# Kernel tuning notes

Measured on AMD Instinct MI355X. Metric: run time of the kernel, lower is better.

Reference implementation:

```python
import jax, jax.numpy as jnp
import numpy as np

B, TM1, ENC, DEC, OUT = 256, 32, 128, 128, 1


def setup_inputs() -> dict:
    key = jax.random.key(0)
    ks = jax.random.split(key, 16)
    s = 0.05
    inp = {
        "input_encoded": jax.random.normal(ks[0], (B, TM1, ENC), jnp.float32),
        "y_history": jax.random.normal(ks[1], (B, TM1, OUT), jnp.float32),
        # attn_layer: Linear(2*DEC+ENC -> ENC), Tanh, Linear(ENC -> 1)
        "attn_W1": jax.random.normal(ks[2], (ENC, 2 * DEC + ENC), jnp.float32) * s,
        "attn_b1": jnp.zeros((ENC,), jnp.float32),
        "attn_W2": jax.random.normal(ks[3], (1, ENC), jnp.float32) * s,
        "attn_b2": jnp.zeros((1,), jnp.float32),
        # LSTM(input_size=OUT, hidden_size=DEC), pytorch gate order i,f,g,o
        "W_ih": jax.random.normal(ks[4], (4 * DEC, OUT), jnp.float32) * s,
        "W_hh": jax.random.normal(ks[5], (4 * DEC, DEC), jnp.float32) * s,
        "b_ih": jnp.zeros((4 * DEC,), jnp.float32),
        "b_hh": jnp.zeros((4 * DEC,), jnp.float32),
        # fc: Linear(ENC+OUT -> OUT), weight initialized with normal_() in torch
        "fc_W": jax.random.normal(ks[6], (OUT, ENC + OUT), jnp.float32),
        "fc_b": jnp.zeros((OUT,), jnp.float32),
        # fc_final: Linear(DEC+ENC -> OUT)
        "fcf_W": jax.random.normal(ks[7], (OUT, DEC + ENC), jnp.float32) * s,
        "fcf_b": jnp.zeros((OUT,), jnp.float32),
    }
    return inp


def _forward(input_encoded, y_history, attn_W1, attn_b1, attn_W2, attn_b2,
             W_ih, W_hh, b_ih, b_hh, fc_W, fc_b, fcf_W, fcf_b):
    b, tm1, enc = input_encoded.shape
    dec = W_hh.shape[1]

    h0 = jnp.zeros((b, dec), input_encoded.dtype)
    c0 = jnp.zeros((b, dec), input_encoded.dtype)
    ctx0 = jnp.zeros((b, enc), input_encoded.dtype)

    def step(carry, y_t):  # y_t: [B, OUT]
        h, c, _ = carry
        hc = jnp.concatenate([h, c], axis=-1)  # [B, 2*DEC]
        x = jnp.concatenate(
            [jnp.broadcast_to(hc[:, None, :], (b, tm1, 2 * dec)), input_encoded],
            axis=-1)  # [B, T-1, 2*DEC+ENC]
        hdn = jnp.tanh(jnp.einsum('bte,he->bth', x, attn_W1) + attn_b1)
        logits = jnp.einsum('bth,oh->bto', hdn, attn_W2)[..., 0] + attn_b2[0]  # [B, T-1]
        attn = jax.nn.softmax(logits, axis=1)
        ctx = jnp.einsum('bt,bte->be', attn, input_encoded)  # [B, ENC]
        y_tilde = jnp.concatenate([ctx, y_t], axis=1) @ fc_W.T + fc_b  # [B, OUT]
        gates = y_tilde @ W_ih.T + b_ih + h @ W_hh.T + b_hh  # [B, 4*DEC]
        i, f, g, o = jnp.split(gates, 4, axis=-1)
        c_new = jax.nn.sigmoid(f) * c + jax.nn.sigmoid(i) * jnp.tanh(g)
        h_new = jax.nn.sigmoid(o) * jnp.tanh(c_new)
        return (h_new, c_new, ctx), None

    (h, c, ctx), _ = jax.lax.scan(step, (h0, c0, ctx0),
                                  jnp.swapaxes(y_history, 0, 1))
    out = jnp.concatenate([h, ctx], axis=1) @ fcf_W.T + fcf_b + y_history[:, -1]
    return out  # [B, OUT]


def reference(input_encoded, y_history, attn_W1, attn_b1, attn_W2, attn_b2,
              W_ih, W_hh, b_ih, b_hh, fc_W, fc_b, fcf_W, fcf_b):
    return _forward(input_encoded, y_history, attn_W1, attn_b1, attn_W2, attn_b2,
                    W_ih, W_hh, b_ih, b_hh, fc_W, fc_b, fcf_W, fcf_b)
```

## Files before the change

### kernel.cpp

```cpp
#include <hip/hip_runtime.h>


#define TT 32

typedef _Float16 h2_t __attribute__((ext_vector_type(2)));
typedef _Float16 h4_t __attribute__((ext_vector_type(4)));
typedef _Float16 h8_t __attribute__((ext_vector_type(8)));

#if __has_builtin(__builtin_amdgcn_fdot2)
#define FDOT2(a, b, c) __builtin_amdgcn_fdot2((a), (b), (c), false)
#else
static __device__ __forceinline__ float FDOT2(h2_t a, h2_t b, float c) {
    return c + (float)a[0] * (float)b[0] + (float)a[1] * (float)b[1];
}
#endif

__device__ __forceinline__ float dot_h8(h8_t w, h8_t v, float acc) {
    acc = FDOT2(__builtin_shufflevector(w, w, 0, 1), __builtin_shufflevector(v, v, 0, 1), acc);
    acc = FDOT2(__builtin_shufflevector(w, w, 2, 3), __builtin_shufflevector(v, v, 2, 3), acc);
    acc = FDOT2(__builtin_shufflevector(w, w, 4, 5), __builtin_shufflevector(v, v, 4, 5), acc);
    acc = FDOT2(__builtin_shufflevector(w, w, 6, 7), __builtin_shufflevector(v, v, 6, 7), acc);
    return acc;
}
__device__ __forceinline__ h8_t pk8(float4 a, float4 b) {
    h8_t r;
    r[0] = (_Float16)a.x; r[1] = (_Float16)a.y; r[2] = (_Float16)a.z; r[3] = (_Float16)a.w;
    r[4] = (_Float16)b.x; r[5] = (_Float16)b.y; r[6] = (_Float16)b.z; r[7] = (_Float16)b.w;
    return r;
}
__device__ __forceinline__ float fast_tanh(float x) {
    float e = __expf(2.f * x);
    return 1.f - __fdividef(2.f, e + 1.f);
}
__device__ __forceinline__ float fast_sig(float x) {
    return __fdividef(1.f, 1.f + __expf(-x));
}

__global__ __launch_bounds__(1024, 4) void decoder_kernel(
    const float* __restrict__ enc_g,
    const float* __restrict__ yh_g,
    const float* __restrict__ W1,
    const float* __restrict__ b1,
    const float* __restrict__ W2,
    const float* __restrict__ b2,
    const float* __restrict__ Wih,
    const float* __restrict__ Whh,
    const float* __restrict__ bih,
    const float* __restrict__ bhh,
    const float* __restrict__ fcW,
    const float* __restrict__ fcB,
    const float* __restrict__ fcfW,
    const float* __restrict__ fcfB,
    float* __restrict__ out)
{
    __shared__ __align__(16) h8_t s_whh8[512 * 16];
    __shared__ __align__(16) _Float16 s_enc16[TT * 136];
    __shared__ __align__(16) _Float16 s_epre16[TT * 128];
    __shared__ __align__(16) _Float16 s_hcx[4 * 272];
    __shared__ __align__(16) _Float16 s_A16[128];
    __shared__ __align__(16) _Float16 s_w216[128];
    __shared__ __align__(16) float s_gdot[512];
    __shared__ __align__(16) _Float16 s_wih16[512];
    __shared__ float s_logit[TT];
    __shared__ float s_q[TT];
    __shared__ float s_att[TT];
    __shared__ float s_yh[TT];
    __shared__ float s_ctx[128];

    const int tid = threadIdx.x;
    const int b = blockIdx.x;
    const int lane = tid & 63;

    {
        const float4* encp = (const float4*)(enc_g + (size_t)b * TT * 128);
        float4 v = encp[tid];
        int t = tid >> 5, e4 = tid & 31;
        h4_t hv;
        hv[0] = (_Float16)v.x; hv[1] = (_Float16)v.y;
        hv[2] = (_Float16)v.z; hv[3] = (_Float16)v.w;
        *(h4_t*)(s_enc16 + t * 136 + e4 * 4) = hv;
    }
    if (tid < 544) ((unsigned int*)s_hcx)[tid] = 0u;
    if (tid < 128) s_w216[tid] = (_Float16)W2[tid];
    if (tid < TT) s_yh[tid] = yh_g[b * TT + tid];

    float bias_r = 0.f;
    h8_t w1a[8];
    if (tid < 512) {
        const int r = tid, rx = r & 15;
        const float4* wp = (const float4*)(Whh + (size_t)r * 128);
#pragma unroll
        for (int c = 0; c < 16; c++)
            s_whh8[(r << 4) | (c ^ rx)] = pk8(wp[2 * c], wp[2 * c + 1]);
        s_wih16[r] = (_Float16)Wih[r];
        bias_r = bih[r] + bhh[r];
    } else {
        const int u = tid - 512, g = u >> 2, s4 = u & 3;
        const float4* p = (const float4*)(W1 + g * 384 + s4 * 64);
#pragma unroll
        for (int k = 0; k < 8; k++) w1a[k] = pk8(p[2 * k], p[2 * k + 1]);
    }
    const float b2v = b2[0];
    const float fcw128 = fcW[128];
    const float fcbv = fcB[0];
    const float fcfbv = fcfB[0];
    __syncthreads();

    {
        const int g8 = tid >> 3, s8 = tid & 7;
        const float4* wp = (const float4*)(W1 + g8 * 384 + 256 + s8 * 16);
        h8_t wa = pk8(wp[0], wp[1]);
        h8_t wb = pk8(wp[2], wp[3]);
        const float b1v = b1[g8];
        for (int t = 0; t < TT; t++) {
            const h8_t* ep8 = (const h8_t*)(s_enc16 + t * 136);
            float pa = dot_h8(wa, ep8[s8 * 2], 0.f);
            pa = dot_h8(wb, ep8[s8 * 2 + 1], pa);
            pa += __shfl_xor(pa, 1);
            pa += __shfl_xor(pa, 2);
            pa += __shfl_xor(pa, 4);
            if (s8 == 0) s_epre16[t * 128 + g8] = (_Float16)(pa + b1v);
        }
    }
    if (tid < 256) {
        const int t = tid >> 3, s8 = tid & 7;
        const float4* fp = (const float4*)(fcW + s8 * 16);
        h8_t fa = pk8(fp[0], fp[1]);
        h8_t fb = pk8(fp[2], fp[3]);
        const h8_t* ep8 = (const h8_t*)(s_enc16 + t * 136);
        float pq = dot_h8(fa, ep8[s8 * 2], 0.f);
        pq = dot_h8(fb, ep8[s8 * 2 + 1], pq);
        pq += __shfl_xor(pq, 1);
        pq += __shfl_xor(pq, 2);
        pq += __shfl_xor(pq, 4);
        if (s8 == 0) s_q[t] = pq;
    }
    h8_t w8wih;
    float c0r = 0.f, c1r = 0.f;
    if (tid >= 512 && tid < 576) {
#pragma unroll
        for (int j = 0; j < 8; j++) w8wih[j] = s_wih16[j * 64 + lane];
    }
    __syncthreads();

    const h8_t* hcp8 = (const h8_t*)s_hcx;

#define GDOT(c, acc) acc = dot_h8(s_whh8[base | ((c) ^ rx)], hcp8[(c)], acc)

    for (int t = 0; t < TT; t++) {
        float pg0 = 0.f, pg1 = 0.f;
        if (tid < 512) {
            const int rx = tid & 15, base = tid << 4;
            GDOT(0, pg0); GDOT(1, pg1); GDOT(2, pg0); GDOT(3, pg1);
            GDOT(4, pg0); GDOT(5, pg1); GDOT(6, pg0); GDOT(7, pg1);
        } else {
            const int u = tid - 512, g = u >> 2, s4 = u & 3;
            const h8_t* hp = (const h8_t*)(s_hcx + s4 * 272);
            float a0 = 0.f, a1 = 0.f;
#pragma unroll
            for (int k = 0; k < 8; k += 2) {
                a0 = dot_h8(w1a[k], hp[s4 * 8 + k], a0);
                a1 = dot_h8(w1a[k + 1], hp[s4 * 8 + k + 1], a1);
            }
            float aa = a0 + a1;
            aa += __shfl_xor(aa, 1);
            aa += __shfl_xor(aa, 2);
            if (s4 == 0) s_A16[g] = (_Float16)aa;
        }
        __syncthreads();

        if (tid < 512) {
            const int rx = tid & 15, base = tid << 4;
            GDOT(8, pg0); GDOT(9, pg1); GDOT(10, pg0); GDOT(11, pg1);
            GDOT(12, pg0); GDOT(13, pg1); GDOT(14, pg0); GDOT(15, pg1);
            s_gdot[tid] = pg0 + pg1 + bias_r;
        } else {
            const int u = tid - 512, tt_ = u >> 4, sub = u & 15;
            h8_t ev = ((const h8_t*)(s_epre16 + tt_ * 128))[sub];
            h8_t av = ((const h8_t*)s_A16)[sub];
            h8_t wv = ((const h8_t*)s_w216)[sub];
            float lp = 0.f;
#pragma unroll
            for (int i = 0; i < 8; i++)
                lp += (float)wv[i] * fast_tanh((float)av[i] + (float)ev[i]);
            lp += __shfl_xor(lp, 1);
            lp += __shfl_xor(lp, 2);
            lp += __shfl_xor(lp, 4);
            lp += __shfl_xor(lp, 8);
            if (sub == 0) s_logit[tt_] = lp + b2v;
        }
        __syncthreads();

        if (tid >= 512 && tid < 576) {
            float el = 0.f, ql = 0.f;
            if (lane < TT) { el = __expf(s_logit[lane]); ql = s_q[lane]; }
            float ss = el, ys = el * ql;
#pragma unroll
            for (int m = 1; m < 64; m <<= 1) {
                ss += __shfl_xor(ss, m);
                ys += __shfl_xor(ys, m);
            }
            float inv = __fdividef(1.f, ss);
            if (lane < TT) s_att[lane] = el * inv;
            float yt = ys * inv + fcw128 * s_yh[t] + fcbv;
            float g0 = s_gdot[lane]       + (float)w8wih[0] * yt;
            float g1 = s_gdot[64 + lane]  + (float)w8wih[1] * yt;
            float g2 = s_gdot[128 + lane] + (float)w8wih[2] * yt;
            float g3 = s_gdot[192 + lane] + (float)w8wih[3] * yt;
            float g4 = s_gdot[256 + lane] + (float)w8wih[4] * yt;
            float g5 = s_gdot[320 + lane] + (float)w8wih[5] * yt;
            float g6 = s_gdot[384 + lane] + (float)w8wih[6] * yt;
            float g7 = s_gdot[448 + lane] + (float)w8wih[7] * yt;
            float cn0 = fast_sig(g2) * c0r + fast_sig(g0) * fast_tanh(g4);
            float cn1 = fast_sig(g3) * c1r + fast_sig(g1) * fast_tanh(g5);
            float hn0 = fast_sig(g6) * fast_tanh(cn0);
            float hn1 = fast_sig(g7) * fast_tanh(cn1);
            c0r = cn0; c1r = cn1;
            _Float16 h0 = (_Float16)hn0, h1 = (_Float16)hn1;
            _Float16 cc0 = (_Float16)cn0, cc1 = (_Float16)cn1;
#pragma unroll
            for (int j = 0; j < 4; j++) {
                _Float16* bp = s_hcx + j * 272;
                bp[lane] = h0;
                bp[64 + lane] = h1;
                bp[128 + lane] = cc0;
                bp[192 + lane] = cc1;
            }
        }
        __syncthreads();
    }
#undef GDOT

    if (tid < 128) {
        float acc = 0.f;
#pragma unroll 8
        for (int t = 0; t < TT; t++) acc += s_att[t] * (float)s_enc16[t * 136 + tid];
        s_ctx[tid] = acc;
    }
    __syncthreads();
    if (tid < 64) {
        float p = fcfW[lane] * (float)s_hcx[lane] +
                  fcfW[64 + lane] * (float)s_hcx[64 + lane] +
                  fcfW[128 + lane] * s_ctx[lane] +
                  fcfW[192 + lane] * s_ctx[64 + lane];
#pragma unroll
        for (int m = 1; m < 64; m <<= 1) p += __shfl_xor(p, m);
        if (lane == 0) out[b] = p + fcfbv + s_yh[TT - 1];
    }
}

extern "C" void kernel_launch(void* const* d_in, const int* in_sizes, int n_in,
                              void* d_out, int out_size, void* d_ws, size_t ws_size,
                              hipStream_t stream) {
    decoder_kernel<<<256, 1024, 0, stream>>>(
        (const float*)d_in[0], (const float*)d_in[1], (const float*)d_in[2],
        (const float*)d_in[3], (const float*)d_in[4], (const float*)d_in[5],
        (const float*)d_in[6], (const float*)d_in[7], (const float*)d_in[8],
        (const float*)d_in[9], (const float*)d_in[10], (const float*)d_in[11],
        (const float*)d_in[12], (const float*)d_in[13], (float*)d_out);
}
```

Before: 173.8 us.

## Halve block size, keep W_hh in registers, spread LSTM gate activations

Measured after the change: 173.6 us. About the same (-0.1%).

```diff
diff --git a/kernel.cpp b/kernel.cpp
--- a/kernel.cpp
+++ b/kernel.cpp
@@ -36,7 +36,7 @@
     return __fdividef(1.f, 1.f + __expf(-x));
 }
 
-__global__ __launch_bounds__(1024, 4) void decoder_kernel(
+__global__ __launch_bounds__(512, 2) void decoder_kernel(
     const float* __restrict__ enc_g,
     const float* __restrict__ yh_g,
     const float* __restrict__ W1,
@@ -53,14 +53,13 @@
     const float* __restrict__ fcfB,
     float* __restrict__ out)
 {
-    __shared__ __align__(16) h8_t s_whh8[512 * 16];
+    __shared__ __align__(16) h8_t s_w1a8[512 * 8];
     __shared__ __align__(16) _Float16 s_enc16[TT * 136];
     __shared__ __align__(16) _Float16 s_epre16[TT * 128];
-    __shared__ __align__(16) _Float16 s_hcx[4 * 272];
+    __shared__ __align__(16) _Float16 s_hc[2 * 272];
     __shared__ __align__(16) _Float16 s_A16[128];
     __shared__ __align__(16) _Float16 s_w216[128];
-    __shared__ __align__(16) float s_gdot[512];
-    __shared__ __align__(16) _Float16 s_wih16[512];
+    __shared__ __align__(16) float s_act[512];
     __shared__ float s_logit[TT];
     __shared__ float s_q[TT];
     __shared__ float s_att[TT];
@@ -70,35 +69,40 @@
     const int tid = threadIdx.x;
     const int b = blockIdx.x;
     const int lane = tid & 63;
+    const int g1 = tid >> 2, s4 = tid & 3;
+    const int rx7 = tid & 7;
 
     {
         const float4* encp = (const float4*)(enc_g + (size_t)b * TT * 128);
-        float4 v = encp[tid];
-        int t = tid >> 5, e4 = tid & 31;
-        h4_t hv;
-        hv[0] = (_Float16)v.x; hv[1] = (_Float16)v.y;
-        hv[2] = (_Float16)v.z; hv[3] = (_Float16)v.w;
-        *(h4_t*)(s_enc16 + t * 136 + e4 * 4) = hv;
-    }
-    if (tid < 544) ((unsigned int*)s_hcx)[tid] = 0u;
+#pragma unroll
+        for (int r = 0; r < 2; r++) {
+            int gi = tid * 2 + r;
+            float4 v = encp[gi];
+            int t = gi >> 5, e4 = gi & 31;
+            h4_t hv;
+            hv[0] = (_Float16)v.x; hv[1] = (_Float16)v.y;
+            hv[2] = (_Float16)v.z; hv[3] = (_Float16)v.w;
+            *(h4_t*)(s_enc16 + t * 136 + e4 * 4) = hv;
+        }
+    }
+    if (tid < 272) ((unsigned int*)s_hc)[tid] = 0u;
     if (tid < 128) s_w216[tid] = (_Float16)W2[tid];
     if (tid < TT) s_yh[tid] = yh_g[b * TT + tid];
 
-    float bias_r = 0.f;
-    h8_t w1a[8];
-    if (tid < 512) {
-        const int r = tid, rx = r & 15;
-        const float4* wp = (const float4*)(Whh + (size_t)r * 128);
-#pragma unroll
-        for (int c = 0; c < 16; c++)
-            s_whh8[(r << 4) | (c ^ rx)] = pk8(wp[2 * c], wp[2 * c + 1]);
-        s_wih16[r] = (_Float16)Wih[r];
-        bias_r = bih[r] + bhh[r];
-    } else {
-        const int u = tid - 512, g = u >> 2, s4 = u & 3;
-        const float4* p = (const float4*)(W1 + g * 384 + s4 * 64);
-#pragma unroll
-        for (int k = 0; k < 8; k++) w1a[k] = pk8(p[2 * k], p[2 * k + 1]);
+    h8_t whhreg[16];
+    {
+        const float4* wp = (const float4*)(Whh + (size_t)tid * 128);
+#pragma unroll
+        for (int k = 0; k < 16; k++) whhreg[k] = pk8(wp[2 * k], wp[2 * k + 1]);
+    }
+    const float wih_r = Wih[tid];
+    const float bias_r = bih[tid] + bhh[tid];
+
+    {
+        const float4* p = (const float4*)(W1 + g1 * 384 + s4 * 64);
+#pragma unroll
+        for (int k = 0; k < 8; k++)
+            s_w1a8[tid * 8 + (k ^ rx7)] = pk8(p[2 * k], p[2 * k + 1]);
     }
     const float b2v = b2[0];
     const float fcw128 = fcW[128];
@@ -107,75 +111,81 @@
     __syncthreads();
 
     {
-        const int g8 = tid >> 3, s8 = tid & 7;
-        const float4* wp = (const float4*)(W1 + g8 * 384 + 256 + s8 * 16);
-        h8_t wa = pk8(wp[0], wp[1]);
-        h8_t wb = pk8(wp[2], wp[3]);
-        const float b1v = b1[g8];
+        const float4* wp = (const float4*)(W1 + g1 * 384 + 256 + s4 * 32);
+        h8_t wa = pk8(wp[0], wp[1]), wb = pk8(wp[2], wp[3]);
+        h8_t wc = pk8(wp[4], wp[5]), wd = pk8(wp[6], wp[7]);
+        const float b1v = b1[g1];
         for (int t = 0; t < TT; t++) {
             const h8_t* ep8 = (const h8_t*)(s_enc16 + t * 136);
-            float pa = dot_h8(wa, ep8[s8 * 2], 0.f);
-            pa = dot_h8(wb, ep8[s8 * 2 + 1], pa);
-            pa += __shfl_xor(pa, 1);
-            pa += __shfl_xor(pa, 2);
-            pa += __shfl_xor(pa, 4);
-            if (s8 == 0) s_epre16[t * 128 + g8] = (_Float16)(pa + b1v);
-        }
-    }
-    if (tid < 256) {
-        const int t = tid >> 3, s8 = tid & 7;
-        const float4* fp = (const float4*)(fcW + s8 * 16);
-        h8_t fa = pk8(fp[0], fp[1]);
-        h8_t fb = pk8(fp[2], fp[3]);
-        const h8_t* ep8 = (const h8_t*)(s_enc16 + t * 136);
-        float pq = dot_h8(fa, ep8[s8 * 2], 0.f);
-        pq = dot_h8(fb, ep8[s8 * 2 + 1], pq);
+            float pa = dot_h8(wa, ep8[s4 * 4 + 0], 0.f);
+            float pb = dot_h8(wb, ep8[s4 * 4 + 1], 0.f);
+            pa = dot_h8(wc, ep8[s4 * 4 + 2], pa);
+            pb = dot_h8(wd, ep8[s4 * 4 + 3], pb);
+            float pp = pa + pb;
+            pp += __shfl_xor(pp, 1);
+            pp += __shfl_xor(pp, 2);
+            if (s4 == 0) s_epre16[t * 128 + g1] = (_Float16)(pp + b1v);
+        }
+    }
+    if (tid < 128) {
+        const int tq = tid >> 2, sq = tid & 3;
+        const float4* fp = (const float4*)(fcW + sq * 32);
+        h8_t fa = pk8(fp[0], fp[1]), fb = pk8(fp[2], fp[3]);
+        h8_t fc2 = pk8(fp[4], fp[5]), fd = pk8(fp[6], fp[7]);
+        const h8_t* ep8 = (const h8_t*)(s_enc16 + tq * 136);
+        float pa = dot_h8(fa, ep8[sq * 4 + 0], 0.f);
+        float pb = dot_h8(fb, ep8[sq * 4 + 1], 0.f);
+        pa = dot_h8(fc2, ep8[sq * 4 + 2], pa);
+        pb = dot_h8(fd, ep8[sq * 4 + 3], pb);
+        float pq = pa + pb;
         pq += __shfl_xor(pq, 1);
         pq += __shfl_xor(pq, 2);
-        pq += __shfl_xor(pq, 4);
-        if (s8 == 0) s_q[t] = pq;
-    }
-    h8_t w8wih;
-    float c0r = 0.f, c1r = 0.f;
-    if (tid >= 512 && tid < 576) {
-#pragma unroll
-        for (int j = 0; j < 8; j++) w8wih[j] = s_wih16[j * 64 + lane];
-    }
+        if (sq == 0) s_q[tq] = pq;
+    }
+    float c_reg = 0.f;
     __syncthreads();
 
-    const h8_t* hcp8 = (const h8_t*)s_hcx;
-
-#define GDOT(c, acc) acc = dot_h8(s_whh8[base | ((c) ^ rx)], hcp8[(c)], acc)
-
     for (int t = 0; t < TT; t++) {
-        float pg0 = 0.f, pg1 = 0.f;
-        if (tid < 512) {
-            const int rx = tid & 15, base = tid << 4;
-            GDOT(0, pg0); GDOT(1, pg1); GDOT(2, pg0); GDOT(3, pg1);
-            GDOT(4, pg0); GDOT(5, pg1); GDOT(6, pg0); GDOT(7, pg1);
-        } else {
-            const int u = tid - 512, g = u >> 2, s4 = u & 3;
-            const h8_t* hp = (const h8_t*)(s_hcx + s4 * 272);
+        float gdot;
+        {
+            const h8_t* hp = (const h8_t*)s_hc;
+            float a0 = 0.f, a1 = 0.f, a2 = 0.f, a3 = 0.f;
+#pragma unroll
+            for (int k = 0; k < 2; k++) {
+                a0 = dot_h8(whhreg[4 * k + 0], hp[4 * k + 0], a0);
+                a1 = dot_h8(whhreg[4 * k + 1], hp[4 * k + 1], a1);
+                a2 = dot_h8(whhreg[4 * k + 2], hp[4 * k + 2], a2);
+                a3 = dot_h8(whhreg[4 * k + 3], hp[4 * k + 3], a3);
+            }
+            __builtin_amdgcn_sched_barrier(0);
+#pragma unroll
+            for (int k = 2; k < 4; k++) {
+                a0 = dot_h8(whhreg[4 * k + 0], hp[4 * k + 0], a0);
+                a1 = dot_h8(whhreg[4 * k + 1], hp[4 * k + 1], a1);
+                a2 = dot_h8(whhreg[4 * k + 2], hp[4 * k + 2], a2);
+                a3 = dot_h8(whhreg[4 * k + 3], hp[4 * k + 3], a3);
+            }
+            gdot = (a0 + a1) + (a2 + a3) + bias_r;
+        }
+        __builtin_amdgcn_sched_barrier(0);
+        {
+            const h8_t* hcp = (const h8_t*)(s_hc + (s4 >> 1) * 272);
+            const h8_t* wp8 = s_w1a8 + tid * 8;
             float a0 = 0.f, a1 = 0.f;
 #pragma unroll
-            for (int k = 0; k < 8; k += 2) {
-                a0 = dot_h8(w1a[k], hp[s4 * 8 + k], a0);
-                a1 = dot_h8(w1a[k + 1], hp[s4 * 8 + k + 1], a1);
+            for (int k = 0; k < 4; k++) {
+                a0 = dot_h8(wp8[(2 * k) ^ rx7], hcp[s4 * 8 + 2 * k], a0);
+                a1 = dot_h8(wp8[(2 * k + 1) ^ rx7], hcp[s4 * 8 + 2 * k + 1], a1);
             }
             float aa = a0 + a1;
             aa += __shfl_xor(aa, 1);
             aa += __shfl_xor(aa, 2);
-            if (s4 == 0) s_A16[g] = (_Float16)aa;
-        }
-        __syncthreads();
-
-        if (tid < 512) {
-            const int rx = tid & 15, base = tid << 4;
-            GDOT(8, pg0); GDOT(9, pg1); GDOT(10, pg0); GDOT(11, pg1);
-            GDOT(12, pg0); GDOT(13, pg1); GDOT(14, pg0); GDOT(15, pg1);
-            s_gdot[tid] = pg0 + pg1 + bias_r;
-        } else {
-            const int u = tid - 512, tt_ = u >> 4, sub = u & 15;
+            if (s4 == 0) s_A16[g1] = (_Float16)aa;
+        }
+        __syncthreads();
+
+        {
+            const int tt_ = tid >> 4, sub = tid & 15;
             h8_t ev = ((const h8_t*)(s_epre16 + tt_ * 128))[sub];
             h8_t av = ((const h8_t*)s_A16)[sub];
             h8_t wv = ((const h8_t*)s_w216)[sub];
@@ -191,56 +201,51 @@
         }
         __syncthreads();
 
-        if (tid >= 512 && tid < 576) {
-            float el = 0.f, ql = 0.f;
-            if (lane < TT) { el = __expf(s_logit[lane]); ql = s_q[lane]; }
+        float act;
+        {
+            float el = __expf(s_logit[lane & 31]);
+            float ql = s_q[lane & 31];
             float ss = el, ys = el * ql;
 #pragma unroll
-            for (int m = 1; m < 64; m <<= 1) {
+            for (int m = 1; m <= 16; m <<= 1) {
                 ss += __shfl_xor(ss, m);
                 ys += __shfl_xor(ys, m);
             }
             float inv = __fdividef(1.f, ss);
-            if (lane < TT) s_att[lane] = el * inv;
+            if (t == TT - 1 && tid < TT) s_att[tid] = el * inv;
             float yt = ys * inv + fcw128 * s_yh[t] + fcbv;
-            float g0 = s_gdot[lane]       + (float)w8wih[0] * yt;
-            float g1 = s_gdot[64 + lane]  + (float)w8wih[1] * yt;
-            float g2 = s_gdot[128 + lane] + (float)w8wih[2] * yt;
-            float g3 = s_gdot[192 + lane] + (float)w8wih[3] * yt;
-            float g4 = s_gdot[256 + lane] + (float)w8wih[4] * yt;
-            float g5 = s_gdot[320 + lane] + (float)w8wih[5] * yt;
-            float g6 = s_gdot[384 + lane] + (float)w8wih[6] * yt;
-            float g7 = s_gdot[448 + lane] + (float)w8wih[7] * yt;
-            float cn0 = fast_sig(g2) * c0r + fast_sig(g0) * fast_tanh(g4);
-            float cn1 = fast_sig(g3) * c1r + fast_sig(g1) * fast_tanh(g5);
-            float hn0 = fast_sig(g6) * fast_tanh(cn0);
-            float hn1 = fast_sig(g7) * fast_tanh(cn1);
-            c0r = cn0; c1r = cn1;
-            _Float16 h0 = (_Float16)hn0, h1 = (_Float16)hn1;
-            _Float16 cc0 = (_Float16)cn0, cc1 = (_Float16)cn1;
-#pragma unroll
-            for (int j = 0; j < 4; j++) {
-                _Float16* bp = s_hcx + j * 272;
-                bp[lane] = h0;
-                bp[64 + lane] = h1;
-                bp[128 + lane] = cc0;
-                bp[192 + lane] = cc1;
-            }
-        }
-        __syncthreads();
-    }
-#undef GDOT
+            float gv = gdot + wih_r * yt;
+            act = ((tid >> 7) == 2) ? fast_tanh(gv) : fast_sig(gv);
+            s_act[tid] = act;
+        }
+        __syncthreads();
+
+        if (tid < 128) {
+            float af = s_act[128 + tid];
+            float ag = s_act[256 + tid];
+            float ao = s_act[384 + tid];
+            float cn = af * c_reg + act * ag;
+            float hn = ao * fast_tanh(cn);
+            c_reg = cn;
+            _Float16 hh = (_Float16)hn, cc = (_Float16)cn;
+            s_hc[tid] = hh;
+            s_hc[128 + tid] = cc;
+            s_hc[272 + tid] = hh;
+            s_hc[400 + tid] = cc;
+        }
+        __syncthreads();
+    }
 
     if (tid < 128) {
         float acc = 0.f;
 #pragma unroll 8
-        for (int t = 0; t < TT; t++) acc += s_att[t] * (float)s_enc16[t * 136 + tid];
+        for (int t2 = 0; t2 < TT; t2++) acc += s_att[t2] * (float)s_enc16[t2 * 136 + tid];
         s_ctx[tid] = acc;
     }
     __syncthreads();
     if (tid < 64) {
-        float p = fcfW[lane] * (float)s_hcx[lane] +
-                  fcfW[64 + lane] * (float)s_hcx[64 + lane] +
+        float p = fcfW[lane] * (float)s_hc[lane] +
+                  fcfW[64 + lane] * (float)s_hc[64 + lane] +
                   fcfW[128 + lane] * s_ctx[lane] +
                   fcfW[192 + lane] * s_ctx[64 + lane];
 #pragma unroll
@@ -252,7 +257,7 @@
 extern "C" void kernel_launch(void* const* d_in, const int* in_sizes, int n_in,
                               void* d_out, int out_size, void* d_ws, size_t ws_size,
                               hipStream_t stream) {
-    decoder_kernel<<<256, 1024, 0, stream>>>(
+    decoder_kernel<<<256, 512, 0, stream>>>(
         (const float*)d_in[0], (const float*)d_in[1], (const float*)d_in[2],
         (const float*)d_in[3], (const float*)d_in[4], (const float*)d_in[5],
         (const float*)d_in[6], (const float*)d_in[7], (const float*)d_in[8],
```
